# Performance work log

Measured on AMD Instinct MI355X. Metric: run time of the kernel, lower is better.

The kernel has to match this reference:

```python
import jax, jax.numpy as jnp
import numpy as np

D_STATE = 16
DT_RANK = 4


def selective_scan(u, delta, A, Bc, Cc, D):
    """Mamba selective scan.
    u, delta: [S, L, d]; A: [d, N]; Bc, Cc: [S, L, N]; D: [d].
    Returns y: [S, L, d].
    """
    # discretize: deltaA [S,L,d,N], deltaB*u [S,L,d,N]
    dA = jnp.exp(delta[..., None] * A)
    dBu = (delta * u)[..., None] * Bc[:, :, None, :]

    def step(h, inp):
        dA_t, dBu_t, C_t = inp  # [S,d,N], [S,d,N], [S,N]
        h = dA_t * h + dBu_t
        y = jnp.einsum('sdn,sn->sd', h, C_t)
        return h, y

    S, L, d = u.shape
    N = A.shape[1]
    h0 = jnp.zeros((S, d, N), u.dtype)
    _, ys = jax.lax.scan(
        step, h0,
        (dA.transpose(1, 0, 2, 3), dBu.transpose(1, 0, 2, 3), Cc.transpose(1, 0, 2)))
    y = ys.transpose(1, 0, 2)  # [S, L, d]
    return y + u * D


def ssm_branch(u, A_log, D, x_proj_w, dt_proj_w, dt_proj_b):
    """u: [S, L, d] sequence of tokens; applies input-dependent SSM."""
    N = A_log.shape[1]
    proj = jnp.einsum('sld,pd->slp', u, x_proj_w)  # [S,L,dt_rank+2N]
    dt_raw = proj[..., :DT_RANK]
    Bc = proj[..., DT_RANK:DT_RANK + N]
    Cc = proj[..., DT_RANK + N:]
    delta = jax.nn.softplus(jnp.einsum('slr,dr->sld', dt_raw, dt_proj_w) + dt_proj_b)
    A = -jnp.exp(A_log)  # [d, N]
    return selective_scan(u, delta, A, Bc, Cc, D)


def setup_inputs() -> dict:
    key = jax.random.key(0)
    ks = jax.random.split(key, 6)
    B, C, H, W = 4, 64, 128, 128
    x = jax.random.normal(ks[0], (B, C, H, W), jnp.float32)
    A_log = jnp.log(jax.random.uniform(ks[1], (C, D_STATE), jnp.float32, 0.5, 4.0))
    D = jax.random.normal(ks[2], (C,), jnp.float32)
    x_proj_w = jax.random.normal(ks[3], (DT_RANK + 2 * D_STATE, C), jnp.float32) * (C ** -0.5)
    dt_proj_w = jax.random.normal(ks[4], (C, DT_RANK), jnp.float32) * (DT_RANK ** -0.5)
    dt_proj_b = jax.random.normal(ks[5], (C,), jnp.float32) * 0.1
    return {"x": x, "A_log": A_log, "D": D, "x_proj_w": x_proj_w,
            "dt_proj_w": dt_proj_w, "dt_proj_b": dt_proj_b}


def reference(x, A_log, D, x_proj_w, dt_proj_w, dt_proj_b):
    B, C, H, W = x.shape
    # horizontal scan: B*H row-sequences of length W
    u_h = x.transpose(0, 2, 3, 1).reshape(B * H, W, C)
    y_h = ssm_branch(u_h, A_log, D, x_proj_w, dt_proj_w, dt_proj_b)
    y_h = y_h.reshape(B, H, W, C).transpose(0, 3, 1, 2)
    # vertical scan: B*W column-sequences of length H
    u_v = x.transpose(0, 3, 2, 1).reshape(B * W, H, C)
    y_v = ssm_branch(u_v, A_log, D, x_proj_w, dt_proj_w, dt_proj_b)
    y_v = y_v.reshape(B, W, H, C).transpose(0, 3, 2, 1)
    return y_h + y_v
```

## Files before the change

### kernel.cpp

```cpp
#include <hip/hip_runtime.h>

#define BB 4
#define CC 64
#define HH 128
#define WW 128
#define NN 16
#define HW (HH*WW)

__device__ __forceinline__ float softplus_f(float x) {
    float e = __expf(-fabsf(x));
    return fmaxf(x, 0.0f) + __logf(1.0f + e);
}

__global__ __launch_bounds__(256) void k_scan(
    const float* __restrict__ x, const float* __restrict__ xpw,
    const float* __restrict__ A_log, const float* __restrict__ Dv,
    const float* __restrict__ dtw, const float* __restrict__ dtb,
    float* __restrict__ out, float* __restrict__ yv)
{
    __shared__ float xt[64 * 132];
    __shared__ float bc[128 * 36];
    __shared__ float dtr[128 * 4];
    __shared__ float dlt[32 * 64];

    const int t = threadIdx.x;
    const int half = blockIdx.x >> 9;
    const int r9 = blockIdx.x & 511;
    const int b = r9 >> 7;
    const int L = r9 & 127;

    if (half == 0) {
#pragma unroll
        for (int k = 0; k < 8; ++k) {
            int i = k * 256 + t;
            int c = i >> 5, jq = i & 31;
            *(float4*)&xt[c * 132 + jq * 4] =
                *(const float4*)&x[((size_t)(b * CC + c) * HH + L) * WW + jq * 4];
        }
    } else {
#pragma unroll
        for (int p = 0; p < 32; ++p) {
            int i = p * 256 + t;
            int c = i >> 7, j = i & 127;
            xt[c * 132 + j] = x[((size_t)(b * CC + c) * HH + j) * WW + L];
        }
    }
    __syncthreads();

    {
        const int wv = t >> 6, lane = t & 63;
        const int pg2 = __builtin_amdgcn_readfirstlane(wv & 1);
        const int pix = (wv >> 1) * 64 + lane;
        const int p0 = pg2 * 18;
        float acc[18];
#pragma unroll
        for (int j = 0; j < 18; ++j) acc[j] = 0.f;
        for (int c4 = 0; c4 < 16; ++c4) {
            float xv0 = xt[(c4 * 4 + 0) * 132 + pix];
            float xv1 = xt[(c4 * 4 + 1) * 132 + pix];
            float xv2 = xt[(c4 * 4 + 2) * 132 + pix];
            float xv3 = xt[(c4 * 4 + 3) * 132 + pix];
#pragma unroll
            for (int j = 0; j < 18; ++j) {
                float4 wq = *(const float4*)&xpw[(p0 + j) * CC + c4 * 4];
                acc[j] = fmaf(wq.x, xv0, fmaf(wq.y, xv1,
                         fmaf(wq.z, xv2, fmaf(wq.w, xv3, acc[j]))));
            }
        }
        if (pg2 == 0) {
            *(float4*)&dtr[pix * 4] = make_float4(acc[0], acc[1], acc[2], acc[3]);
            *(float4*)&bc[pix * 36 + 4]  = make_float4(acc[4], acc[5], acc[6], acc[7]);
            *(float4*)&bc[pix * 36 + 8]  = make_float4(acc[8], acc[9], acc[10], acc[11]);
            *(float4*)&bc[pix * 36 + 12] = make_float4(acc[12], acc[13], acc[14], acc[15]);
            *(float2*)&bc[pix * 36 + 16] = make_float2(acc[16], acc[17]);
        } else {
            *(float2*)&bc[pix * 36 + 18] = make_float2(acc[0], acc[1]);
            *(float4*)&bc[pix * 36 + 20] = make_float4(acc[2], acc[3], acc[4], acc[5]);
            *(float4*)&bc[pix * 36 + 24] = make_float4(acc[6], acc[7], acc[8], acc[9]);
            *(float4*)&bc[pix * 36 + 28] = make_float4(acc[10], acc[11], acc[12], acc[13]);
            *(float4*)&bc[pix * 36 + 32] = make_float4(acc[14], acc[15], acc[16], acc[17]);
        }
    }
    __syncthreads();

    const int d = t >> 2, ng = t & 3, n0 = ng * 4;
    float A0 = -__expf(A_log[d * NN + n0 + 0]);
    float A1 = -__expf(A_log[d * NN + n0 + 1]);
    float A2 = -__expf(A_log[d * NN + n0 + 2]);
    float A3 = -__expf(A_log[d * NN + n0 + 3]);
    const float Dd = Dv[d];
    float h0 = 0.f, h1 = 0.f, h2 = 0.f, h3 = 0.f;
    const int dd = t & 63, jb = t >> 6;
    const float4 wt4 = *(const float4*)&dtw[dd * 4];
    const float bdd = dtb[dd];
    float* drow = (half == 0 ? out : yv) + ((size_t)(b * CC + d) * 128 + L) * 128;

    for (int ch = 0; ch < 4; ++ch) {
        if (ch) __syncthreads();
#pragma unroll
        for (int k = 0; k < 8; ++k) {
            int jl = jb * 8 + k;
            float4 dr = *(const float4*)&dtr[(ch * 32 + jl) * 4];
            float draw = fmaf(dr.x, wt4.x, fmaf(dr.y, wt4.y,
                         fmaf(dr.z, wt4.z, fmaf(dr.w, wt4.w, bdd))));
            dlt[jl * 64 + dd] = softplus_f(draw);
        }
        __syncthreads();
        float yb[8];
        for (int jo = 0; jo < 4; ++jo) {
#pragma unroll
            for (int uu = 0; uu < 8; ++uu) {
                const int jl = jo * 8 + uu;
                const int j = ch * 32 + jl;
                float delta = dlt[jl * 64 + d];
                float u = xt[d * 132 + j];
                float4 Bv = *(const float4*)&bc[j * 36 + 4 + n0];
                float4 Cv = *(const float4*)&bc[j * 36 + 20 + n0];
                float du = delta * u;
                h0 = fmaf(__expf(delta * A0), h0, du * Bv.x);
                h1 = fmaf(__expf(delta * A1), h1, du * Bv.y);
                h2 = fmaf(__expf(delta * A2), h2, du * Bv.z);
                h3 = fmaf(__expf(delta * A3), h3, du * Bv.w);
                float y = fmaf(h0, Cv.x, fmaf(h1, Cv.y,
                          fmaf(h2, Cv.z, h3 * Cv.w)));
                y += __shfl_xor(y, 1);
                y += __shfl_xor(y, 2);
                y = fmaf(u, Dd, y);
                if (ng == jo) yb[uu] = y;
            }
        }
        *(float4*)&drow[ch * 32 + ng * 8]     = make_float4(yb[0], yb[1], yb[2], yb[3]);
        *(float4*)&drow[ch * 32 + ng * 8 + 4] = make_float4(yb[4], yb[5], yb[6], yb[7]);
    }
}

__global__ __launch_bounds__(256) void k_add(const float* __restrict__ yv,
                                             float* __restrict__ out)
{
    __shared__ float td[32 * 33];
    int t = threadIdx.x;
    int bc_ = blockIdx.x >> 4;
    int tb = blockIdx.x & 15;
    int w0 = (tb & 3) * 32;
    int h0 = (tb >> 2) * 32;
    const float* src = yv + (size_t)bc_ * HW;
    float* dst = out + (size_t)bc_ * HW;
    int r = t >> 3, q = t & 7;
    float4 v = *(const float4*)&src[(w0 + r) * HH + h0 + q * 4];
    td[r * 33 + q * 4 + 0] = v.x;
    td[r * 33 + q * 4 + 1] = v.y;
    td[r * 33 + q * 4 + 2] = v.z;
    td[r * 33 + q * 4 + 3] = v.w;
    __syncthreads();
    float* op = &dst[(h0 + r) * WW + w0 + q * 4];
    float4 o = *(float4*)op;
    o.x += td[(q * 4 + 0) * 33 + r];
    o.y += td[(q * 4 + 1) * 33 + r];
    o.z += td[(q * 4 + 2) * 33 + r];
    o.w += td[(q * 4 + 3) * 33 + r];
    *(float4*)op = o;
}

extern "C" void kernel_launch(void* const* d_in, const int* in_sizes, int n_in,
                              void* d_out, int out_size, void* d_ws, size_t ws_size,
                              hipStream_t stream) {
    const float* x     = (const float*)d_in[0];
    const float* A_log = (const float*)d_in[1];
    const float* Dv    = (const float*)d_in[2];
    const float* xpw   = (const float*)d_in[3];
    const float* dtw   = (const float*)d_in[4];
    const float* dtb   = (const float*)d_in[5];
    float* out = (float*)d_out;
    float* yv  = (float*)d_ws;

    k_scan<<<1024, 256, 0, stream>>>(x, xpw, A_log, Dv, dtw, dtb, out, yv);
    k_add <<<BB * CC * 16, 256, 0, stream>>>(yv, out);
}
```

Measured before the change: 156.0 us.

## Swizzle shared-memory layouts and shrink delta chunk to cut LDS use

Changes the xt tile to a pixel-major layout with a rotating channel swizzle, and stores the B/C projections in a 32-float row with an XOR swizzle of float4 slots, to avoid LDS bank conflicts and reduce padding. The delta chunk shrinks from 32 to 8 timesteps, giving 16 chunks with smaller dlt storage, and outputs are written as float2 per chunk instead of float4 pairs. Total shared memory drops, which may allow more blocks per CU. In exchange there are more barriers per block, narrower global stores, and the vertical-half gather now writes scalar swizzled addresses. One barrier after the projection is removed and covered by the barrier at the start of the chunk loop.

```diff
diff --git a/kernel.cpp b/kernel.cpp
--- a/kernel.cpp
+++ b/kernel.cpp
@@ -18,10 +18,10 @@
     const float* __restrict__ dtw, const float* __restrict__ dtb,
     float* __restrict__ out, float* __restrict__ yv)
 {
-    __shared__ float xt[64 * 132];
-    __shared__ float bc[128 * 36];
+    __shared__ float xt[128 * 64];
+    __shared__ float bcs[128 * 32];
     __shared__ float dtr[128 * 4];
-    __shared__ float dlt[32 * 64];
+    __shared__ float dlt[8 * 64];
 
     const int t = threadIdx.x;
     const int half = blockIdx.x >> 9;
@@ -34,15 +34,19 @@
         for (int k = 0; k < 8; ++k) {
             int i = k * 256 + t;
             int c = i >> 5, jq = i & 31;
-            *(float4*)&xt[c * 132 + jq * 4] =
-                *(const float4*)&x[((size_t)(b * CC + c) * HH + L) * WW + jq * 4];
+            float4 v = *(const float4*)&x[((size_t)(b * CC + c) * HH + L) * WW + jq * 4];
+            int j0 = jq * 4;
+            xt[(j0 + 0) * 64 + ((c + j0 + 0) & 63)] = v.x;
+            xt[(j0 + 1) * 64 + ((c + j0 + 1) & 63)] = v.y;
+            xt[(j0 + 2) * 64 + ((c + j0 + 2) & 63)] = v.z;
+            xt[(j0 + 3) * 64 + ((c + j0 + 3) & 63)] = v.w;
         }
     } else {
 #pragma unroll
         for (int p = 0; p < 32; ++p) {
-            int i = p * 256 + t;
-            int c = i >> 7, j = i & 127;
-            xt[c * 132 + j] = x[((size_t)(b * CC + c) * HH + j) * WW + L];
+            int c = t & 63, j = p * 4 + (t >> 6);
+            xt[j * 64 + ((c + j) & 63)] =
+                x[((size_t)(b * CC + c) * HH + j) * WW + L];
         }
     }
     __syncthreads();
@@ -52,14 +56,15 @@
         const int pg2 = __builtin_amdgcn_readfirstlane(wv & 1);
         const int pix = (wv >> 1) * 64 + lane;
         const int p0 = pg2 * 18;
+        const int sw = pix & 7;
         float acc[18];
 #pragma unroll
         for (int j = 0; j < 18; ++j) acc[j] = 0.f;
         for (int c4 = 0; c4 < 16; ++c4) {
-            float xv0 = xt[(c4 * 4 + 0) * 132 + pix];
-            float xv1 = xt[(c4 * 4 + 1) * 132 + pix];
-            float xv2 = xt[(c4 * 4 + 2) * 132 + pix];
-            float xv3 = xt[(c4 * 4 + 3) * 132 + pix];
+            float xv0 = xt[pix * 64 + ((c4 * 4 + 0 + pix) & 63)];
+            float xv1 = xt[pix * 64 + ((c4 * 4 + 1 + pix) & 63)];
+            float xv2 = xt[pix * 64 + ((c4 * 4 + 2 + pix) & 63)];
+            float xv3 = xt[pix * 64 + ((c4 * 4 + 3 + pix) & 63)];
 #pragma unroll
             for (int j = 0; j < 18; ++j) {
                 float4 wq = *(const float4*)&xpw[(p0 + j) * CC + c4 * 4];
@@ -67,21 +72,23 @@
                          fmaf(wq.z, xv2, fmaf(wq.w, xv3, acc[j]))));
             }
         }
+        float* bp = &bcs[pix * 32];
         if (pg2 == 0) {
             *(float4*)&dtr[pix * 4] = make_float4(acc[0], acc[1], acc[2], acc[3]);
-            *(float4*)&bc[pix * 36 + 4]  = make_float4(acc[4], acc[5], acc[6], acc[7]);
-            *(float4*)&bc[pix * 36 + 8]  = make_float4(acc[8], acc[9], acc[10], acc[11]);
-            *(float4*)&bc[pix * 36 + 12] = make_float4(acc[12], acc[13], acc[14], acc[15]);
-            *(float2*)&bc[pix * 36 + 16] = make_float2(acc[16], acc[17]);
+            *(float4*)&bp[((0 ^ sw) << 2)] = make_float4(acc[4], acc[5], acc[6], acc[7]);
+            *(float4*)&bp[((1 ^ sw) << 2)] = make_float4(acc[8], acc[9], acc[10], acc[11]);
+            *(float4*)&bp[((2 ^ sw) << 2)] = make_float4(acc[12], acc[13], acc[14], acc[15]);
+            bp[((3 ^ sw) << 2) + 0] = acc[16];
+            bp[((3 ^ sw) << 2) + 1] = acc[17];
         } else {
-            *(float2*)&bc[pix * 36 + 18] = make_float2(acc[0], acc[1]);
-            *(float4*)&bc[pix * 36 + 20] = make_float4(acc[2], acc[3], acc[4], acc[5]);
-            *(float4*)&bc[pix * 36 + 24] = make_float4(acc[6], acc[7], acc[8], acc[9]);
-            *(float4*)&bc[pix * 36 + 28] = make_float4(acc[10], acc[11], acc[12], acc[13]);
-            *(float4*)&bc[pix * 36 + 32] = make_float4(acc[14], acc[15], acc[16], acc[17]);
+            bp[((3 ^ sw) << 2) + 2] = acc[0];
+            bp[((3 ^ sw) << 2) + 3] = acc[1];
+            *(float4*)&bp[((4 ^ sw) << 2)] = make_float4(acc[2], acc[3], acc[4], acc[5]);
+            *(float4*)&bp[((5 ^ sw) << 2)] = make_float4(acc[6], acc[7], acc[8], acc[9]);
+            *(float4*)&bp[((6 ^ sw) << 2)] = make_float4(acc[10], acc[11], acc[12], acc[13]);
+            *(float4*)&bp[((7 ^ sw) << 2)] = make_float4(acc[14], acc[15], acc[16], acc[17]);
         }
     }
-    __syncthreads();
 
     const int d = t >> 2, ng = t & 3, n0 = ng * 4;
     float A0 = -__expf(A_log[d * NN + n0 + 0]);
@@ -95,42 +102,38 @@
     const float bdd = dtb[dd];
     float* drow = (half == 0 ? out : yv) + ((size_t)(b * CC + d) * 128 + L) * 128;
 
-    for (int ch = 0; ch < 4; ++ch) {
-        if (ch) __syncthreads();
+    for (int ch = 0; ch < 16; ++ch) {
+        __syncthreads();
 #pragma unroll
-        for (int k = 0; k < 8; ++k) {
-            int jl = jb * 8 + k;
-            float4 dr = *(const float4*)&dtr[(ch * 32 + jl) * 4];
+        for (int k = 0; k < 2; ++k) {
+            int jl = jb * 2 + k;
+            float4 dr = *(const float4*)&dtr[(ch * 8 + jl) * 4];
             float draw = fmaf(dr.x, wt4.x, fmaf(dr.y, wt4.y,
                          fmaf(dr.z, wt4.z, fmaf(dr.w, wt4.w, bdd))));
             dlt[jl * 64 + dd] = softplus_f(draw);
         }
         __syncthreads();
-        float yb[8];
-        for (int jo = 0; jo < 4; ++jo) {
+        float y0 = 0.f, y1 = 0.f;
 #pragma unroll
-            for (int uu = 0; uu < 8; ++uu) {
-                const int jl = jo * 8 + uu;
-                const int j = ch * 32 + jl;
-                float delta = dlt[jl * 64 + d];
-                float u = xt[d * 132 + j];
-                float4 Bv = *(const float4*)&bc[j * 36 + 4 + n0];
-                float4 Cv = *(const float4*)&bc[j * 36 + 20 + n0];
-                float du = delta * u;
-                h0 = fmaf(__expf(delta * A0), h0, du * Bv.x);
-                h1 = fmaf(__expf(delta * A1), h1, du * Bv.y);
-                h2 = fmaf(__expf(delta * A2), h2, du * Bv.z);
-                h3 = fmaf(__expf(delta * A3), h3, du * Bv.w);
-                float y = fmaf(h0, Cv.x, fmaf(h1, Cv.y,
-                          fmaf(h2, Cv.z, h3 * Cv.w)));
-                y += __shfl_xor(y, 1);
-                y += __shfl_xor(y, 2);
-                y = fmaf(u, Dd, y);
-                if (ng == jo) yb[uu] = y;
-            }
+        for (int jl = 0; jl < 8; ++jl) {
+            const int j = ch * 8 + jl;
+            float delta = dlt[jl * 64 + d];
+            float u = xt[j * 64 + ((d + j) & 63)];
+            const int s = j & 7;
+            float4 Bv = *(const float4*)&bcs[j * 32 + ((ng ^ s) << 2)];
+            float4 Cv = *(const float4*)&bcs[j * 32 + (((4 + ng) ^ s) << 2)];
+            float du = delta * u;
+            h0 = fmaf(__expf(delta * A0), h0, du * Bv.x);
+            h1 = fmaf(__expf(delta * A1), h1, du * Bv.y);
+            h2 = fmaf(__expf(delta * A2), h2, du * Bv.z);
+            h3 = fmaf(__expf(delta * A3), h3, du * Bv.w);
+            float y = fmaf(h0, Cv.x, fmaf(h1, Cv.y, fmaf(h2, Cv.z, h3 * Cv.w)));
+            y += __shfl_xor(y, 1);
+            y += __shfl_xor(y, 2);
+            y = fmaf(u, Dd, y);
+            if (ng == (jl >> 1)) { if (jl & 1) y1 = y; else y0 = y; }
         }
-        *(float4*)&drow[ch * 32 + ng * 8]     = make_float4(yb[0], yb[1], yb[2], yb[3]);
-        *(float4*)&drow[ch * 32 + ng * 8 + 4] = make_float4(yb[4], yb[5], yb[6], yb[7]);
+        *(float2*)&drow[ch * 8 + ng * 2] = make_float2(y0, y1);
     }
 }
 
```

New measurement: 150.5 us. -3.6%, faster.
